# Kernel tuning notes

Hardware: AMD Instinct MI355X
Metric: run time of the kernel (lower is better)

The kernel has to match this reference:

```python
import jax, jax.numpy as jnp
import numpy as np

B, D, H = 1024, 64, 128


def setup_inputs() -> dict:
    key = jax.random.key(0)
    ks = jax.random.split(key, 12)
    s1 = 1.0 / np.sqrt(4 * D)
    sh = 1.0 / np.sqrt(H)
    sd = 1.0 / np.sqrt(D)
    return {
        "x": jax.random.normal(ks[0], (B, D), dtype=jnp.float32),
        # edge_fn: Linear(4D,H) -> ReLU -> Linear(H,H)
        "W1": jax.random.uniform(ks[1], (4 * D, H), minval=-s1, maxval=s1, dtype=jnp.float32),
        "b1": jax.random.uniform(ks[2], (H,), minval=-s1, maxval=s1, dtype=jnp.float32),
        "W2": jax.random.uniform(ks[3], (H, H), minval=-sh, maxval=sh, dtype=jnp.float32),
        "b2": jax.random.uniform(ks[4], (H,), minval=-sh, maxval=sh, dtype=jnp.float32),
        # tau_proj: Linear(D,1) -> Softplus
        "Wt": jax.random.uniform(ks[5], (D, 1), minval=-sd, maxval=sd, dtype=jnp.float32),
        "bt": jax.random.uniform(ks[6], (1,), minval=-sd, maxval=sd, dtype=jnp.float32),
        # agg: Linear(H,H) -> ReLU
        "Wa": jax.random.uniform(ks[7], (H, H), minval=-sh, maxval=sh, dtype=jnp.float32),
        "ba": jax.random.uniform(ks[8], (H,), minval=-sh, maxval=sh, dtype=jnp.float32),
        # res_proj: Linear(D,H)
        "Wr": jax.random.uniform(ks[9], (D, H), minval=-sd, maxval=sd, dtype=jnp.float32),
        "br": jax.random.uniform(ks[10], (H,), minval=-sd, maxval=sd, dtype=jnp.float32),
        # LayerNorm(H)
        "gamma": jnp.ones((H,), dtype=jnp.float32),
        "beta": jnp.zeros((H,), dtype=jnp.float32),
    }


def reference(x, W1, b1, W2, b2, Wt, bt, Wa, ba, Wr, br, gamma, beta):
    d = x.shape[1]
    # Decompose first linear over concat([x_i, x_j, delta, |delta|]) into 4 sub-matmuls;
    # only the |delta| term needs the pairwise [B,B,D] tensor.
    Wi, Wj, Wd, Wab = W1[:d], W1[d:2 * d], W1[2 * d:3 * d], W1[3 * d:]
    ti = x @ Wi            # [B,H] (i-dependent)
    tj = x @ Wj            # [B,H] (j-dependent)
    td = x @ Wd            # [B,H] (delta = x_i - x_j contribution)
    delta = x[:, None, :] - x[None, :, :]             # [B,B,D]
    ta = jnp.einsum('ijd,dh->ijh', jnp.abs(delta), Wab)  # [B,B,H]
    pre = ti[:, None, :] + tj[None, :, :] + td[:, None, :] - td[None, :, :] + ta + b1
    d_proj = jax.nn.relu(pre) @ W2 + b2               # [B,B,H]
    tau = jnp.maximum(jax.nn.softplus(x @ Wt + bt), 0.01) + 1.0  # [B,1]
    h_mean = d_proj.mean(axis=1) / tau                # mean over j
    h = jax.nn.relu(h_mean @ Wa + ba)
    y = h + (x @ Wr + br)
    mu = y.mean(axis=-1, keepdims=True)
    var = ((y - mu) ** 2).mean(axis=-1, keepdims=True)  # biased, like torch LayerNorm
    return (y - mu) * jax.lax.rsqrt(var + 1e-5) * gamma + beta
```

## Files before the change

### kernel.cpp

```cpp
#include <hip/hip_runtime.h>
#include <hip/hip_bf16.h>
#include <math.h>

#define BB 1024
#define DD 64
#define HH 128

typedef __bf16 bf16x8 __attribute__((ext_vector_type(8)));
typedef float floatx4 __attribute__((ext_vector_type(4)));

__device__ __forceinline__ unsigned short f2bf(float v) {
    union { float f; unsigned u; } a; a.f = v;
    unsigned r = a.u + 0x7fffu + ((a.u >> 16) & 1u);
    return (unsigned short)(r >> 16);
}

__device__ __forceinline__ void async_cp16(const float* g, float* lds_wave_base) {
    __builtin_amdgcn_global_load_lds(
        (const __attribute__((address_space(1))) unsigned int*)g,
        (__attribute__((address_space(3))) unsigned int*)lds_wave_base,
        16, 0, 0);
}

__global__ __launch_bounds__(256) void prep_kernel(
    const float* __restrict__ x, const float* __restrict__ W1,
    const float* __restrict__ b1,
    float* __restrict__ c1, float* __restrict__ c2P,
    unsigned short* __restrict__ wpack)
{
    __shared__ float xr[2][DD];
    const int t = threadIdx.x;
    const int i0 = blockIdx.x * 2;
    if (t < 2 * DD) xr[t >> 6][t & 63] = x[i0 * DD + t];
    __syncthreads();

    const int ii = t >> 7, h = t & 127;
    const int i = i0 + ii;
    float a1 = 0.f, a2 = 0.f;
    #pragma unroll 16
    for (int k = 0; k < DD; k++) {
        float wi = W1[k * HH + h];
        float wj = W1[(DD + k) * HH + h];
        float wd = W1[(2 * DD + k) * HH + h];
        float xv = xr[ii][k];
        a1 = fmaf(xv, wi + wd, a1);
        a2 = fmaf(xv, wj - wd, a2);
    }
    c1[i * HH + h] = a1 + b1[h];
    const int jl = i & 15;
    c2P[(i >> 4) * 2048 + (h >> 4) * 256 + (((jl >> 2) << 4) | (h & 15)) * 4 + (jl & 3)] = a2;

    if (blockIdx.x == 0) {
        for (int f = t; f < 16384; f += 256) {
            int jj = f & 7, l = (f >> 3) & 63, u = f >> 9;
            int s = u & 1, t8 = u >> 1;
            int k = s * 32 + ((l >> 4) << 3) + jj;
            int hh = t8 * 16 + (l & 15);
            wpack[f] = f2bf(W1[(3 * DD + k) * HH + hh]);
        }
    }
}

__global__ __launch_bounds__(256) void pair_kernel(
    const float* __restrict__ x, const float* __restrict__ c1,
    const float* __restrict__ c2P, const unsigned short* __restrict__ wpack,
    float* __restrict__ Sp)
{
    __shared__ __align__(16) float xs[2][16][DD];
    __shared__ __align__(16) float c2s[2][2048];

    const int t = threadIdx.x;
    const int wave = t >> 6;
    const int l = t & 63;
    const int quad = l >> 4, lm = l & 15;
    const int ig = blockIdx.x >> 2;
    const int jq = blockIdx.x & 3;
    const int i = ig * 4 + wave;
    const int j0base = jq * 256;

    {
        async_cp16(x + (j0base + (t >> 4)) * DD + (t & 15) * 4,
                   &xs[0][0][0] + wave * 256);
        const float* cg = c2P + (j0base >> 4) * 2048;
        async_cp16(cg + t * 4,        &c2s[0][0]    + wave * 256);
        async_cp16(cg + 1024 + t * 4, &c2s[0][1024] + wave * 256);
    }

    float xi[16];
    {
        const float* xrg = x + i * DD + quad * 8;
        *(float4*)(xi)      = *(const float4*)(xrg);
        *(float4*)(xi + 4)  = *(const float4*)(xrg + 4);
        *(float4*)(xi + 8)  = *(const float4*)(xrg + 32);
        *(float4*)(xi + 12) = *(const float4*)(xrg + 36);
    }
    float c1r[8];
    #pragma unroll
    for (int t8 = 0; t8 < 8; t8++) c1r[t8] = c1[i * HH + t8 * 16 + lm];
    bf16x8 wf[16];
    #pragma unroll
    for (int u = 0; u < 16; u++)
        wf[u] = *(const bf16x8*)(wpack + (u * 64 + l) * 8);

    float S[8];
    #pragma unroll
    for (int t8 = 0; t8 < 8; t8++) S[t8] = 0.f;

    for (int tile = 0; tile < 16; ++tile) {
        const int cur = tile & 1;
        __syncthreads();

        if (tile < 15) {
            const int jn = j0base + (tile + 1) * 16;
            const int nb = cur ^ 1;
            async_cp16(x + (jn + (t >> 4)) * DD + (t & 15) * 4,
                       &xs[nb][0][0] + wave * 256);
            const float* cg = c2P + (jn >> 4) * 2048;
            async_cp16(cg + t * 4,        &c2s[nb][0]    + wave * 256);
            async_cp16(cg + 1024 + t * 4, &c2s[nb][1024] + wave * 256);
        }

        const float* xrow = &xs[cur][lm][quad * 8];
        float4 a0 = *(const float4*)(xrow);
        float4 a1 = *(const float4*)(xrow + 4);
        float4 a2 = *(const float4*)(xrow + 32);
        float4 a3 = *(const float4*)(xrow + 36);
        bf16x8 af0, af1;
        af0[0] = (__bf16)fabsf(xi[0] - a0.x);  af0[1] = (__bf16)fabsf(xi[1] - a0.y);
        af0[2] = (__bf16)fabsf(xi[2] - a0.z);  af0[3] = (__bf16)fabsf(xi[3] - a0.w);
        af0[4] = (__bf16)fabsf(xi[4] - a1.x);  af0[5] = (__bf16)fabsf(xi[5] - a1.y);
        af0[6] = (__bf16)fabsf(xi[6] - a1.z);  af0[7] = (__bf16)fabsf(xi[7] - a1.w);
        af1[0] = (__bf16)fabsf(xi[8] - a2.x);  af1[1] = (__bf16)fabsf(xi[9] - a2.y);
        af1[2] = (__bf16)fabsf(xi[10] - a2.z); af1[3] = (__bf16)fabsf(xi[11] - a2.w);
        af1[4] = (__bf16)fabsf(xi[12] - a3.x); af1[5] = (__bf16)fabsf(xi[13] - a3.y);
        af1[6] = (__bf16)fabsf(xi[14] - a3.z); af1[7] = (__bf16)fabsf(xi[15] - a3.w);

        floatx4 acc[8];
        #pragma unroll
        for (int t8 = 0; t8 < 8; t8++) {
            acc[t8][0] = c1r[t8]; acc[t8][1] = c1r[t8];
            acc[t8][2] = c1r[t8]; acc[t8][3] = c1r[t8];
        }
        #pragma unroll
        for (int t8 = 0; t8 < 8; t8++) {
            acc[t8] = __builtin_amdgcn_mfma_f32_16x16x32_bf16(af0, wf[t8 * 2 + 0], acc[t8], 0, 0, 0);
            acc[t8] = __builtin_amdgcn_mfma_f32_16x16x32_bf16(af1, wf[t8 * 2 + 1], acc[t8], 0, 0, 0);
        }
        #pragma unroll
        for (int t8 = 0; t8 < 8; t8++) {
            float4 c2v = *(const float4*)(&c2s[cur][t8 * 256 + l * 4]);
            S[t8] += fmaxf(acc[t8][0] + c2v.x, 0.f);
            S[t8] += fmaxf(acc[t8][1] + c2v.y, 0.f);
            S[t8] += fmaxf(acc[t8][2] + c2v.z, 0.f);
            S[t8] += fmaxf(acc[t8][3] + c2v.w, 0.f);
        }
    }

    #pragma unroll
    for (int t8 = 0; t8 < 8; t8++) {
        S[t8] += __shfl_xor(S[t8], 16, 64);
        S[t8] += __shfl_xor(S[t8], 32, 64);
    }
    if (quad == 0) {
        #pragma unroll
        for (int t8 = 0; t8 < 8; t8++)
            Sp[(jq * BB + i) * HH + t8 * 16 + lm] = S[t8];
    }
}

__global__ __launch_bounds__(256) void finish_kernel(
    const float* __restrict__ Sp, const float* __restrict__ W2,
    const float* __restrict__ b2, const float* __restrict__ x,
    const float* __restrict__ Wt, const float* __restrict__ bt,
    const float* __restrict__ Wa, const float* __restrict__ ba,
    const float* __restrict__ Wr, const float* __restrict__ br,
    const float* __restrict__ gamma, const float* __restrict__ beta,
    float* __restrict__ out)
{
    __shared__ float Srow[2][HH];
    __shared__ float mrow[2][HH];
    __shared__ float xrow[2][DD];
    __shared__ float taus[2];
    __shared__ float red1[2][2];
    __shared__ float red2[2][2];
    const int t = threadIdx.x;
    const int ii = t >> 7, h = t & 127;
    const int i = blockIdx.x * 2 + ii;

    float s = 0.f;
    #pragma unroll
    for (int q = 0; q < 4; q++) s += Sp[(q * BB + i) * HH + h];
    Srow[ii][h] = s * (1.0f / (float)BB);
    if (h < 64) xrow[ii][h] = x[i * DD + h];

    if ((t & 127) < 64) {
        int lane = t & 63;
        float p = x[i * DD + lane] * Wt[lane];
        #pragma unroll
        for (int off = 32; off; off >>= 1) p += __shfl_down(p, off, 64);
        if (lane == 0) {
            float z = p + bt[0];
            float sp = (z > 20.f) ? z : log1pf(expf(z));
            taus[ii] = fmaxf(sp, 0.01f) + 1.0f;
        }
    }
    __syncthreads();

    float acc = b2[h];
    #pragma unroll 8
    for (int k = 0; k < HH; k++) acc += Srow[ii][k] * W2[k * HH + h];
    float mv = acc / taus[ii];
    mrow[ii][h] = mv;
    __syncthreads();

    float acc2 = ba[h];
    #pragma unroll 8
    for (int k = 0; k < HH; k++) acc2 += mrow[ii][k] * Wa[k * HH + h];
    float y = fmaxf(acc2, 0.f) + br[h];
    #pragma unroll 8
    for (int d = 0; d < DD; d++) y += xrow[ii][d] * Wr[d * HH + h];

    const int wv = (t >> 6) & 1;
    const int lane = t & 63;
    float p = y;
    #pragma unroll
    for (int off = 32; off; off >>= 1) p += __shfl_down(p, off, 64);
    if (lane == 0) red1[ii][wv] = p;
    __syncthreads();
    float mu = (red1[ii][0] + red1[ii][1]) * (1.f / (float)HH);
    float dy = y - mu;
    float q = dy * dy;
    #pragma unroll
    for (int off = 32; off; off >>= 1) q += __shfl_down(q, off, 64);
    if (lane == 0) red2[ii][wv] = q;
    __syncthreads();
    float var = (red2[ii][0] + red2[ii][1]) * (1.f / (float)HH);
    out[i * HH + h] = dy * rsqrtf(var + 1e-5f) * gamma[h] + beta[h];
}

extern "C" void kernel_launch(void* const* d_in, const int* in_sizes, int n_in,
                              void* d_out, int out_size, void* d_ws, size_t ws_size,
                              hipStream_t stream)
{
    const float* x     = (const float*)d_in[0];
    const float* W1    = (const float*)d_in[1];
    const float* b1    = (const float*)d_in[2];
    const float* W2    = (const float*)d_in[3];
    const float* b2    = (const float*)d_in[4];
    const float* Wt    = (const float*)d_in[5];
    const float* bt    = (const float*)d_in[6];
    const float* Wa    = (const float*)d_in[7];
    const float* ba    = (const float*)d_in[8];
    const float* Wr    = (const float*)d_in[9];
    const float* br    = (const float*)d_in[10];
    const float* gamma = (const float*)d_in[11];
    const float* beta  = (const float*)d_in[12];
    float* out = (float*)d_out;

    char* ws = (char*)d_ws;
    float*          c1    = (float*)(ws);
    float*          c2P   = (float*)(ws + (512 << 10));
    unsigned short* wpack = (unsigned short*)(ws + (1024 << 10));
    float*          Sp    = (float*)(ws + (1056 << 10));

    prep_kernel<<<512, 256, 0, stream>>>(x, W1, b1, c1, c2P, wpack);
    pair_kernel<<<1024, 256, 0, stream>>>(x, c1, c2P, wpack, Sp);
    finish_kernel<<<BB / 2, 256, 0, stream>>>(Sp, W2, b2, x, Wt, bt,
                                              Wa, ba, Wr, br, gamma, beta, out);
}
```

Before: 146.4 us.

## Process two i rows per wave, 32-row j tiles with swizzled LDS

Each wave now handles two i rows, so every x_j tile and c2 tile loaded into LDS feeds twice the MFMA work and the grid shrinks to 512 blocks. The j tile grows to 32 rows with an XOR swizzle on the x tile to avoid LDS bank conflicts, and launch bounds ask for two blocks per SM. The wpack bf16 conversion in the prep kernel is spread across 64 blocks instead of one serial block. The cost is more registers per thread (two accumulator sets, two xi/c1 copies) and fewer blocks for latency hiding.

After: 246.2 us. 1.68x slower.

```diff
diff --git a/kernel.cpp b/kernel.cpp
--- a/kernel.cpp
+++ b/kernel.cpp
@@ -50,24 +50,23 @@
     const int jl = i & 15;
     c2P[(i >> 4) * 2048 + (h >> 4) * 256 + (((jl >> 2) << 4) | (h & 15)) * 4 + (jl & 3)] = a2;
 
-    if (blockIdx.x == 0) {
-        for (int f = t; f < 16384; f += 256) {
-            int jj = f & 7, l = (f >> 3) & 63, u = f >> 9;
-            int s = u & 1, t8 = u >> 1;
-            int k = s * 32 + ((l >> 4) << 3) + jj;
-            int hh = t8 * 16 + (l & 15);
-            wpack[f] = f2bf(W1[(3 * DD + k) * HH + hh]);
-        }
-    }
-}
-
-__global__ __launch_bounds__(256) void pair_kernel(
+    if (blockIdx.x < 64) {
+        int f = blockIdx.x * 256 + t;
+        int jj = f & 7, l = (f >> 3) & 63, u = f >> 9;
+        int s = u & 1, t8 = u >> 1;
+        int k = s * 32 + ((l >> 4) << 3) + jj;
+        int hh = t8 * 16 + (l & 15);
+        wpack[f] = f2bf(W1[(3 * DD + k) * HH + hh]);
+    }
+}
+
+__global__ __launch_bounds__(256, 2) void pair_kernel(
     const float* __restrict__ x, const float* __restrict__ c1,
     const float* __restrict__ c2P, const unsigned short* __restrict__ wpack,
     float* __restrict__ Sp)
 {
-    __shared__ __align__(16) float xs[2][16][DD];
-    __shared__ __align__(16) float c2s[2][2048];
+    __shared__ __align__(16) float xs[2][2048];
+    __shared__ __align__(16) float c2s[2][4096];
 
     const int t = threadIdx.x;
     const int wave = t >> 6;
@@ -75,96 +74,132 @@
     const int quad = l >> 4, lm = l & 15;
     const int ig = blockIdx.x >> 2;
     const int jq = blockIdx.x & 3;
-    const int i = ig * 4 + wave;
+    const int i0 = ig * 8 + wave * 2;
     const int j0base = jq * 256;
 
     {
-        async_cp16(x + (j0base + (t >> 4)) * DD + (t & 15) * 4,
-                   &xs[0][0][0] + wave * 256);
-        const float* cg = c2P + (j0base >> 4) * 2048;
-        async_cp16(cg + t * 4,        &c2s[0][0]    + wave * 256);
-        async_cp16(cg + 1024 + t * 4, &c2s[0][1024] + wave * 256);
-    }
-
-    float xi[16];
-    {
-        const float* xrg = x + i * DD + quad * 8;
-        *(float4*)(xi)      = *(const float4*)(xrg);
-        *(float4*)(xi + 4)  = *(const float4*)(xrg + 4);
-        *(float4*)(xi + 8)  = *(const float4*)(xrg + 32);
-        *(float4*)(xi + 12) = *(const float4*)(xrg + 36);
-    }
-    float c1r[8];
-    #pragma unroll
-    for (int t8 = 0; t8 < 8; t8++) c1r[t8] = c1[i * HH + t8 * 16 + lm];
+        const int j0 = j0base;
+        #pragma unroll
+        for (int p = 0; p < 2; p++) {
+            int j = p * 16 + wave * 4 + quad;
+            int c = lm ^ (j & 7);
+            async_cp16(x + (j0 + j) * DD + c * 4, &xs[0][0] + p * 1024 + wave * 256);
+        }
+        const float* cg = c2P + (j0 >> 4) * 2048;
+        #pragma unroll
+        for (int p = 0; p < 4; p++)
+            async_cp16(cg + (p * 256 + wave * 64 + l) * 4, &c2s[0][0] + p * 1024 + wave * 256);
+    }
+
+    float xi[2][16];
+    #pragma unroll
+    for (int ii = 0; ii < 2; ii++) {
+        const float* xg = x + (i0 + ii) * DD + quad * 8;
+        *(float4*)(xi[ii])      = *(const float4*)(xg);
+        *(float4*)(xi[ii] + 4)  = *(const float4*)(xg + 4);
+        *(float4*)(xi[ii] + 8)  = *(const float4*)(xg + 32);
+        *(float4*)(xi[ii] + 12) = *(const float4*)(xg + 36);
+    }
+    float c1r[2][8];
+    #pragma unroll
+    for (int ii = 0; ii < 2; ii++)
+        #pragma unroll
+        for (int t8 = 0; t8 < 8; t8++)
+            c1r[ii][t8] = c1[(i0 + ii) * HH + t8 * 16 + lm];
     bf16x8 wf[16];
     #pragma unroll
     for (int u = 0; u < 16; u++)
         wf[u] = *(const bf16x8*)(wpack + (u * 64 + l) * 8);
 
-    float S[8];
-    #pragma unroll
-    for (int t8 = 0; t8 < 8; t8++) S[t8] = 0.f;
-
-    for (int tile = 0; tile < 16; ++tile) {
+    float S[2][8];
+    #pragma unroll
+    for (int ii = 0; ii < 2; ii++)
+        #pragma unroll
+        for (int t8 = 0; t8 < 8; t8++) S[ii][t8] = 0.f;
+
+    const int sw = lm & 7;
+
+    for (int tile = 0; tile < 8; ++tile) {
         const int cur = tile & 1;
         __syncthreads();
 
-        if (tile < 15) {
-            const int jn = j0base + (tile + 1) * 16;
+        if (tile < 7) {
+            const int j0 = j0base + (tile + 1) * 32;
             const int nb = cur ^ 1;
-            async_cp16(x + (jn + (t >> 4)) * DD + (t & 15) * 4,
-                       &xs[nb][0][0] + wave * 256);
-            const float* cg = c2P + (jn >> 4) * 2048;
-            async_cp16(cg + t * 4,        &c2s[nb][0]    + wave * 256);
-            async_cp16(cg + 1024 + t * 4, &c2s[nb][1024] + wave * 256);
-        }
-
-        const float* xrow = &xs[cur][lm][quad * 8];
-        float4 a0 = *(const float4*)(xrow);
-        float4 a1 = *(const float4*)(xrow + 4);
-        float4 a2 = *(const float4*)(xrow + 32);
-        float4 a3 = *(const float4*)(xrow + 36);
-        bf16x8 af0, af1;
-        af0[0] = (__bf16)fabsf(xi[0] - a0.x);  af0[1] = (__bf16)fabsf(xi[1] - a0.y);
-        af0[2] = (__bf16)fabsf(xi[2] - a0.z);  af0[3] = (__bf16)fabsf(xi[3] - a0.w);
-        af0[4] = (__bf16)fabsf(xi[4] - a1.x);  af0[5] = (__bf16)fabsf(xi[5] - a1.y);
-        af0[6] = (__bf16)fabsf(xi[6] - a1.z);  af0[7] = (__bf16)fabsf(xi[7] - a1.w);
-        af1[0] = (__bf16)fabsf(xi[8] - a2.x);  af1[1] = (__bf16)fabsf(xi[9] - a2.y);
-        af1[2] = (__bf16)fabsf(xi[10] - a2.z); af1[3] = (__bf16)fabsf(xi[11] - a2.w);
-        af1[4] = (__bf16)fabsf(xi[12] - a3.x); af1[5] = (__bf16)fabsf(xi[13] - a3.y);
-        af1[6] = (__bf16)fabsf(xi[14] - a3.z); af1[7] = (__bf16)fabsf(xi[15] - a3.w);
-
-        floatx4 acc[8];
+            #pragma unroll
+            for (int p = 0; p < 2; p++) {
+                int j = p * 16 + wave * 4 + quad;
+                int c = lm ^ (j & 7);
+                async_cp16(x + (j0 + j) * DD + c * 4, &xs[nb][0] + p * 1024 + wave * 256);
+            }
+            const float* cg = c2P + (j0 >> 4) * 2048;
+            #pragma unroll
+            for (int p = 0; p < 4; p++)
+                async_cp16(cg + (p * 256 + wave * 64 + l) * 4, &c2s[nb][0] + p * 1024 + wave * 256);
+        }
+
+        #pragma unroll
+        for (int st = 0; st < 2; st++) {
+            const float* xb = &xs[cur][0] + (st * 16 + lm) * 16 * 4;
+            float4 a0 = *(const float4*)(xb + ((quad * 2)     ^ sw) * 4);
+            float4 a1 = *(const float4*)(xb + ((quad * 2 + 1) ^ sw) * 4);
+            float4 a2 = *(const float4*)(xb + ((quad * 2 + 8) ^ sw) * 4);
+            float4 a3 = *(const float4*)(xb + ((quad * 2 + 9) ^ sw) * 4);
+
+            floatx4 acc[2][8];
+            #pragma unroll
+            for (int ii = 0; ii < 2; ii++)
+                #pragma unroll
+                for (int t8 = 0; t8 < 8; t8++) {
+                    acc[ii][t8][0] = c1r[ii][t8]; acc[ii][t8][1] = c1r[ii][t8];
+                    acc[ii][t8][2] = c1r[ii][t8]; acc[ii][t8][3] = c1r[ii][t8];
+                }
+
+            #pragma unroll
+            for (int ii = 0; ii < 2; ii++) {
+                bf16x8 af0, af1;
+                af0[0] = (__bf16)fabsf(xi[ii][0] - a0.x);  af0[1] = (__bf16)fabsf(xi[ii][1] - a0.y);
+                af0[2] = (__bf16)fabsf(xi[ii][2] - a0.z);  af0[3] = (__bf16)fabsf(xi[ii][3] - a0.w);
+                af0[4] = (__bf16)fabsf(xi[ii][4] - a1.x);  af0[5] = (__bf16)fabsf(xi[ii][5] - a1.y);
+                af0[6] = (__bf16)fabsf(xi[ii][6] - a1.z);  af0[7] = (__bf16)fabsf(xi[ii][7] - a1.w);
+                af1[0] = (__bf16)fabsf(xi[ii][8] - a2.x);  af1[1] = (__bf16)fabsf(xi[ii][9] - a2.y);
+                af1[2] = (__bf16)fabsf(xi[ii][10] - a2.z); af1[3] = (__bf16)fabsf(xi[ii][11] - a2.w);
+                af1[4] = (__bf16)fabsf(xi[ii][12] - a3.x); af1[5] = (__bf16)fabsf(xi[ii][13] - a3.y);
+                af1[6] = (__bf16)fabsf(xi[ii][14] - a3.z); af1[7] = (__bf16)fabsf(xi[ii][15] - a3.w);
+                #pragma unroll
+                for (int t8 = 0; t8 < 8; t8++) {
+                    acc[ii][t8] = __builtin_amdgcn_mfma_f32_16x16x32_bf16(af0, wf[t8 * 2 + 0], acc[ii][t8], 0, 0, 0);
+                    acc[ii][t8] = __builtin_amdgcn_mfma_f32_16x16x32_bf16(af1, wf[t8 * 2 + 1], acc[ii][t8], 0, 0, 0);
+                }
+            }
+
+            #pragma unroll
+            for (int t8 = 0; t8 < 8; t8++) {
+                float4 c2v = *(const float4*)(&c2s[cur][st * 2048 + t8 * 256 + l * 4]);
+                #pragma unroll
+                for (int ii = 0; ii < 2; ii++) {
+                    S[ii][t8] += fmaxf(acc[ii][t8][0] + c2v.x, 0.f);
+                    S[ii][t8] += fmaxf(acc[ii][t8][1] + c2v.y, 0.f);
+                    S[ii][t8] += fmaxf(acc[ii][t8][2] + c2v.z, 0.f);
+                    S[ii][t8] += fmaxf(acc[ii][t8][3] + c2v.w, 0.f);
+                }
+            }
+        }
+    }
+
+    #pragma unroll
+    for (int ii = 0; ii < 2; ii++)
         #pragma unroll
         for (int t8 = 0; t8 < 8; t8++) {
-            acc[t8][0] = c1r[t8]; acc[t8][1] = c1r[t8];
-            acc[t8][2] = c1r[t8]; acc[t8][3] = c1r[t8];
-        }
-        #pragma unroll
-        for (int t8 = 0; t8 < 8; t8++) {
-            acc[t8] = __builtin_amdgcn_mfma_f32_16x16x32_bf16(af0, wf[t8 * 2 + 0], acc[t8], 0, 0, 0);
-            acc[t8] = __builtin_amdgcn_mfma_f32_16x16x32_bf16(af1, wf[t8 * 2 + 1], acc[t8], 0, 0, 0);
-        }
-        #pragma unroll
-        for (int t8 = 0; t8 < 8; t8++) {
-            float4 c2v = *(const float4*)(&c2s[cur][t8 * 256 + l * 4]);
-            S[t8] += fmaxf(acc[t8][0] + c2v.x, 0.f);
-            S[t8] += fmaxf(acc[t8][1] + c2v.y, 0.f);
-            S[t8] += fmaxf(acc[t8][2] + c2v.z, 0.f);
-            S[t8] += fmaxf(acc[t8][3] + c2v.w, 0.f);
-        }
-    }
-
-    #pragma unroll
-    for (int t8 = 0; t8 < 8; t8++) {
-        S[t8] += __shfl_xor(S[t8], 16, 64);
-        S[t8] += __shfl_xor(S[t8], 32, 64);
-    }
+            S[ii][t8] += __shfl_xor(S[ii][t8], 16, 64);
+            S[ii][t8] += __shfl_xor(S[ii][t8], 32, 64);
+        }
     if (quad == 0) {
         #pragma unroll
-        for (int t8 = 0; t8 < 8; t8++)
-            Sp[(jq * BB + i) * HH + t8 * 16 + lm] = S[t8];
+        for (int ii = 0; ii < 2; ii++)
+            #pragma unroll
+            for (int t8 = 0; t8 < 8; t8++)
+                Sp[(jq * BB + i0 + ii) * HH + t8 * 16 + lm] = S[ii][t8];
     }
 }
 
@@ -264,7 +299,7 @@
     float*          Sp    = (float*)(ws + (1056 << 10));
 
     prep_kernel<<<512, 256, 0, stream>>>(x, W1, b1, c1, c2P, wpack);
-    pair_kernel<<<1024, 256, 0, stream>>>(x, c1, c2P, wpack, Sp);
+    pair_kernel<<<512, 256, 0, stream>>>(x, c1, c2P, wpack, Sp);
     finish_kernel<<<BB / 2, 256, 0, stream>>>(Sp, W2, b2, x, Wt, bt,
                                               Wa, ba, Wr, br, gamma, beta, out);
 }
```

## Load c2 tiles directly from global into accumulators, swizzle x LDS, parallelize wpack

Applied to the files above, without the earlier changes.

The pair kernel no longer stages c2P tiles in LDS. Each lane reads its c2 values straight from global memory and folds them, together with c1, into the MFMA accumulator initial value, which removes the post-MFMA add and about 16 KB of LDS per block. The x tile in LDS now uses an XOR swizzle to avoid bank conflicts on the float4 row reads. The bf16 packing of the W1 |delta| block is spread across 64 prep blocks instead of one serial block. The cost is direct global loads of c2 on the critical path each tile, with latency no longer hidden by the async copy.

Result: faster. 141.5 us (-3.4%).

```diff
diff --git a/kernel.cpp b/kernel.cpp
--- a/kernel.cpp
+++ b/kernel.cpp
@@ -50,14 +50,13 @@
     const int jl = i & 15;
     c2P[(i >> 4) * 2048 + (h >> 4) * 256 + (((jl >> 2) << 4) | (h & 15)) * 4 + (jl & 3)] = a2;
 
-    if (blockIdx.x == 0) {
-        for (int f = t; f < 16384; f += 256) {
-            int jj = f & 7, l = (f >> 3) & 63, u = f >> 9;
-            int s = u & 1, t8 = u >> 1;
-            int k = s * 32 + ((l >> 4) << 3) + jj;
-            int hh = t8 * 16 + (l & 15);
-            wpack[f] = f2bf(W1[(3 * DD + k) * HH + hh]);
-        }
+    if (blockIdx.x < 64) {
+        int f = blockIdx.x * 256 + t;
+        int jj = f & 7, l = (f >> 3) & 63, u = f >> 9;
+        int s = u & 1, t8 = u >> 1;
+        int k = s * 32 + ((l >> 4) << 3) + jj;
+        int hh = t8 * 16 + (l & 15);
+        wpack[f] = f2bf(W1[(3 * DD + k) * HH + hh]);
     }
 }
 
@@ -66,8 +65,7 @@
     const float* __restrict__ c2P, const unsigned short* __restrict__ wpack,
     float* __restrict__ Sp)
 {
-    __shared__ __align__(16) float xs[2][16][DD];
-    __shared__ __align__(16) float c2s[2][2048];
+    __shared__ __align__(16) float xs[2][1024];
 
     const int t = threadIdx.x;
     const int wave = t >> 6;
@@ -77,22 +75,18 @@
     const int jq = blockIdx.x & 3;
     const int i = ig * 4 + wave;
     const int j0base = jq * 256;
-
-    {
-        async_cp16(x + (j0base + (t >> 4)) * DD + (t & 15) * 4,
-                   &xs[0][0][0] + wave * 256);
-        const float* cg = c2P + (j0base >> 4) * 2048;
-        async_cp16(cg + t * 4,        &c2s[0][0]    + wave * 256);
-        async_cp16(cg + 1024 + t * 4, &c2s[0][1024] + wave * 256);
-    }
+    const int sw = lm & 7;
+
+    async_cp16(x + (j0base + (t >> 4)) * DD + (((t & 15) ^ ((t >> 4) & 7)) << 2),
+               &xs[0][0] + wave * 256);
 
     float xi[16];
     {
-        const float* xrg = x + i * DD + quad * 8;
-        *(float4*)(xi)      = *(const float4*)(xrg);
-        *(float4*)(xi + 4)  = *(const float4*)(xrg + 4);
-        *(float4*)(xi + 8)  = *(const float4*)(xrg + 32);
-        *(float4*)(xi + 12) = *(const float4*)(xrg + 36);
+        const float* xg = x + i * DD + quad * 8;
+        *(float4*)(xi)      = *(const float4*)(xg);
+        *(float4*)(xi + 4)  = *(const float4*)(xg + 4);
+        *(float4*)(xi + 8)  = *(const float4*)(xg + 32);
+        *(float4*)(xi + 12) = *(const float4*)(xg + 36);
     }
     float c1r[8];
     #pragma unroll
@@ -112,19 +106,26 @@
 
         if (tile < 15) {
             const int jn = j0base + (tile + 1) * 16;
-            const int nb = cur ^ 1;
-            async_cp16(x + (jn + (t >> 4)) * DD + (t & 15) * 4,
-                       &xs[nb][0][0] + wave * 256);
-            const float* cg = c2P + (jn >> 4) * 2048;
-            async_cp16(cg + t * 4,        &c2s[nb][0]    + wave * 256);
-            async_cp16(cg + 1024 + t * 4, &c2s[nb][1024] + wave * 256);
-        }
-
-        const float* xrow = &xs[cur][lm][quad * 8];
-        float4 a0 = *(const float4*)(xrow);
-        float4 a1 = *(const float4*)(xrow + 4);
-        float4 a2 = *(const float4*)(xrow + 32);
-        float4 a3 = *(const float4*)(xrow + 36);
+            async_cp16(x + (jn + (t >> 4)) * DD + (((t & 15) ^ ((t >> 4) & 7)) << 2),
+                       &xs[cur ^ 1][0] + wave * 256);
+        }
+
+        const float* cg = c2P + ((j0base + tile * 16) >> 4) * 2048;
+        floatx4 acc[8];
+        #pragma unroll
+        for (int t8 = 0; t8 < 8; t8++) {
+            float4 c2v = *(const float4*)(cg + t8 * 256 + l * 4);
+            acc[t8][0] = c2v.x + c1r[t8];
+            acc[t8][1] = c2v.y + c1r[t8];
+            acc[t8][2] = c2v.z + c1r[t8];
+            acc[t8][3] = c2v.w + c1r[t8];
+        }
+
+        const float* xb = &xs[cur][lm * 64];
+        float4 a0 = *(const float4*)(xb + (((quad * 2)     ^ sw) << 2));
+        float4 a1 = *(const float4*)(xb + (((quad * 2 + 1) ^ sw) << 2));
+        float4 a2 = *(const float4*)(xb + (((quad * 2 + 8) ^ sw) << 2));
+        float4 a3 = *(const float4*)(xb + (((quad * 2 + 9) ^ sw) << 2));
         bf16x8 af0, af1;
         af0[0] = (__bf16)fabsf(xi[0] - a0.x);  af0[1] = (__bf16)fabsf(xi[1] - a0.y);
         af0[2] = (__bf16)fabsf(xi[2] - a0.z);  af0[3] = (__bf16)fabsf(xi[3] - a0.w);
@@ -135,12 +136,6 @@
         af1[4] = (__bf16)fabsf(xi[12] - a3.x); af1[5] = (__bf16)fabsf(xi[13] - a3.y);
         af1[6] = (__bf16)fabsf(xi[14] - a3.z); af1[7] = (__bf16)fabsf(xi[15] - a3.w);
 
-        floatx4 acc[8];
-        #pragma unroll
-        for (int t8 = 0; t8 < 8; t8++) {
-            acc[t8][0] = c1r[t8]; acc[t8][1] = c1r[t8];
-            acc[t8][2] = c1r[t8]; acc[t8][3] = c1r[t8];
-        }
         #pragma unroll
         for (int t8 = 0; t8 < 8; t8++) {
             acc[t8] = __builtin_amdgcn_mfma_f32_16x16x32_bf16(af0, wf[t8 * 2 + 0], acc[t8], 0, 0, 0);
@@ -148,11 +143,10 @@
         }
         #pragma unroll
         for (int t8 = 0; t8 < 8; t8++) {
-            float4 c2v = *(const float4*)(&c2s[cur][t8 * 256 + l * 4]);
-            S[t8] += fmaxf(acc[t8][0] + c2v.x, 0.f);
-            S[t8] += fmaxf(acc[t8][1] + c2v.y, 0.f);
-            S[t8] += fmaxf(acc[t8][2] + c2v.z, 0.f);
-            S[t8] += fmaxf(acc[t8][3] + c2v.w, 0.f);
+            S[t8] += fmaxf(acc[t8][0], 0.f);
+            S[t8] += fmaxf(acc[t8][1], 0.f);
+            S[t8] += fmaxf(acc[t8][2], 0.f);
+            S[t8] += fmaxf(acc[t8][3], 0.f);
         }
     }
 
```
